# Optimization experiments

Hardware: AMD Instinct MI355X
Metric: run time of the kernel (lower is better)

## Reference

```python
import jax, jax.numpy as jnp
import numpy as np

HIDDEN = 384
HEADS = 8
DIM_HEAD = HIDDEN // HEADS  # 48
INNER = DIM_HEAD * HEADS
SCALE = DIM_HEAD ** -0.5


def setup_inputs() -> dict:
    key = jax.random.key(0)
    k1, k2, k3, k4 = jax.random.split(key, 4)
    B, C, D, H, W = 2, HIDDEN, 16, 16, 8
    x = jax.random.normal(k1, (B, C, D, H, W), dtype=jnp.float32)
    # nn.Linear weights (stored as [out, in] in torch; use [in, out] here)
    w_qkv = jax.random.normal(k2, (C, 3 * INNER), dtype=jnp.float32) * (C ** -0.5)
    w_out = jax.random.normal(k3, (INNER, C), dtype=jnp.float32) * (INNER ** -0.5)
    b_out = jax.random.normal(k4, (C,), dtype=jnp.float32) * 0.02
    return {"x": x, "w_qkv": w_qkv, "w_out": w_out, "b_out": b_out}


def reference(x, w_qkv, w_out, b_out):
    B, C, D, H, W = x.shape
    N = D * H * W
    tokens = x.reshape(B, C, N).transpose(0, 2, 1)          # [B, N, C]
    qkv = tokens @ w_qkv                                     # [B, N, 3*inner]
    qkv = qkv.reshape(B, N, 3, HEADS, DIM_HEAD).transpose(2, 0, 3, 1, 4)
    q, k, v = qkv[0], qkv[1], qkv[2]                         # [B, h, N, dh]
    q = jnp.clip(q, -5.0, 5.0)
    k = jnp.clip(k, -5.0, 5.0)
    logits = jnp.einsum('bhnd,bhmd->bhnm', q, k) * SCALE     # [B, h, N, N]
    logits = logits - jnp.max(logits, axis=-1, keepdims=True)
    attn = jax.nn.softmax(logits, axis=-1)
    out = jnp.einsum('bhnm,bhmd->bhnd', attn, v)             # [B, h, N, dh]
    out = out.transpose(0, 2, 1, 3).reshape(B, N, INNER)     # [B, N, inner]
    out = out @ w_out + b_out                                # [B, N, C]
    out = out.transpose(0, 2, 1).reshape(B, C, D, H, W)
    return x + out
```

## Files before the change

kernel.cpp:

```cpp
#include <hip/hip_runtime.h>

#define B_SZ 2
#define C_IN 384
#define N_TOK 2048
#define HEADS 8
#define DH 48
#define J3 1152
#define ATTN_SCALE 0.14433756729740643f

typedef __attribute__((ext_vector_type(8))) _Float16 f16x8;
typedef __attribute__((ext_vector_type(4))) _Float16 f16x4;
typedef __attribute__((ext_vector_type(4))) float f32x4;

__device__ __forceinline__ unsigned short f2h(float f) {
  _Float16 h = (_Float16)f;
  return __builtin_bit_cast(unsigned short, h);
}
__device__ __forceinline__ uint pk2(float a, float b) {
  return __builtin_bit_cast(uint, __builtin_amdgcn_cvt_pkrtz(a, b));
}

__global__ __launch_bounds__(256) void tr_kernel(
    const float* __restrict__ x, const float* __restrict__ wq,
    const float* __restrict__ wo, unsigned short* __restrict__ xh,
    unsigned short* __restrict__ wqh, unsigned short* __restrict__ woh) {
  const int z = blockIdx.z;
  const float* src;
  unsigned short* dst;
  int C;
  if (z < 2) {
    src = x + (size_t)z * C_IN * N_TOK;
    dst = xh + (size_t)z * N_TOK * C_IN;
    C = N_TOK;
  } else if (z == 2) {
    src = wq; dst = wqh; C = J3;
  } else {
    src = wo; dst = woh; C = C_IN;
  }
  const int c0 = blockIdx.x * 64;
  const int r0 = blockIdx.y * 64;
  if (c0 >= C) return;
  __shared__ unsigned short T[64][74];
  const int tid = threadIdx.x;
  const int cc = tid & 63;
#pragma unroll
  for (int i = 0; i < 16; ++i) {
    const int rr = 4 * i + (tid >> 6);
    T[cc][rr] = f2h(src[(size_t)(r0 + rr) * C + c0 + cc]);
  }
  __syncthreads();
  const int cc2 = tid >> 2;
  const int seg = (tid & 3) * 16;
  uint v[8];
#pragma unroll
  for (int k = 0; k < 8; ++k)
    v[k] = (uint)T[cc2][seg + 2 * k] | ((uint)T[cc2][seg + 2 * k + 1] << 16);
  unsigned short* dp = dst + (size_t)(c0 + cc2) * C_IN + r0 + seg;
  *(uint4*)dp = make_uint4(v[0], v[1], v[2], v[3]);
  *(uint4*)(dp + 8) = make_uint4(v[4], v[5], v[6], v[7]);
}

__global__ __launch_bounds__(256) void qkv_mfma(
    const unsigned short* __restrict__ xh, const unsigned short* __restrict__ wqh,
    unsigned short* __restrict__ Qo, unsigned short* __restrict__ Ko,
    unsigned short* __restrict__ Vo) {
  __shared__ __align__(16) unsigned short Ts[128][72];
  __shared__ __align__(16) unsigned short Ws[64][72];
  const int tid = threadIdx.x;
  const int w = tid >> 6, lane = tid & 63;
  const int lc = lane & 15, lg = lane >> 4;
  const int m0 = blockIdx.x * 128;
  const int j0 = blockIdx.y * 64;
  const int b = m0 >> 11;

  f32x4 acc[2][4];
#pragma unroll
  for (int i = 0; i < 2; ++i)
#pragma unroll
    for (int j = 0; j < 4; ++j) acc[i][j] = (f32x4){0.f, 0.f, 0.f, 0.f};

  const int trow = tid & 127, tseg = tid >> 7;
  const int wrow = tid & 63,  wseg = tid >> 6;

  for (int kk = 0; kk < C_IN; kk += 64) {
    {
      const uint4* s = (const uint4*)(xh + (size_t)(m0 + trow) * C_IN + kk + tseg * 32);
      uint4* d = (uint4*)&Ts[trow][tseg * 32];
      d[0] = s[0]; d[1] = s[1]; d[2] = s[2]; d[3] = s[3];
      const uint4* s2 = (const uint4*)(wqh + (size_t)(j0 + wrow) * C_IN + kk + wseg * 16);
      uint4* d2 = (uint4*)&Ws[wrow][wseg * 16];
      d2[0] = s2[0]; d2[1] = s2[1];
    }
    __syncthreads();
    f16x8 a[2][2], bf[4][2];
#pragma unroll
    for (int mt = 0; mt < 2; ++mt)
#pragma unroll
      for (int kh = 0; kh < 2; ++kh)
        a[mt][kh] = *(const f16x8*)&Ts[32 * w + 16 * mt + lc][32 * kh + 8 * lg];
#pragma unroll
    for (int jt = 0; jt < 4; ++jt)
#pragma unroll
      for (int kh = 0; kh < 2; ++kh)
        bf[jt][kh] = *(const f16x8*)&Ws[16 * jt + lc][32 * kh + 8 * lg];
#pragma unroll
    for (int mt = 0; mt < 2; ++mt)
#pragma unroll
      for (int jt = 0; jt < 4; ++jt)
#pragma unroll
        for (int kh = 0; kh < 2; ++kh)
          acc[mt][jt] = __builtin_amdgcn_mfma_f32_16x16x32_f16(a[mt][kh], bf[jt][kh], acc[mt][jt], 0, 0, 0);
    __syncthreads();
  }

#pragma unroll
  for (int jt = 0; jt < 4; ++jt) {
    const int jlo = j0 + 16 * jt;
    const int which = jlo / 384;
    const int rr = jlo - which * 384;
    const int head = rr / DH;
    const int dbase = rr - head * DH;
    const int d = dbase + lc;
    const int bh = b * HEADS + head;
#pragma unroll
    for (int mt = 0; mt < 2; ++mt)
#pragma unroll
      for (int r = 0; r < 4; ++r) {
        const int n = (m0 + 32 * w + 16 * mt + 4 * lg + r) & 2047;
        float val = acc[mt][jt][r];
        if (which == 0) {
          val = fminf(fmaxf(val, -5.f), 5.f) * ATTN_SCALE;
          Qo[((size_t)bh * N_TOK + n) * DH + d] = f2h(val);
        } else if (which == 1) {
          val = fminf(fmaxf(val, -5.f), 5.f);
          Ko[((size_t)bh * N_TOK + n) * DH + d] = f2h(val);
        } else {
          Vo[((size_t)bh * DH + d) * N_TOK + n] = f2h(val);
        }
      }
  }
}

__global__ __launch_bounds__(512) void attn_kernel(
    const unsigned short* __restrict__ Q, const unsigned short* __restrict__ K,
    const unsigned short* __restrict__ Vt, unsigned short* __restrict__ Opart,
    float2* __restrict__ ml) {
  const int qt = blockIdx.x, bh = blockIdx.y, ks = blockIdx.z;
  const int b = bh >> 3, h = bh & 7;
  const int n0 = qt * 128;
  const int tid = threadIdx.x;
  const int w = tid >> 6, lane = tid & 63;
  const int lc = lane & 15, lg = lane >> 4;

  __shared__ __align__(16) unsigned short Ks[64][56];
  __shared__ __align__(16) unsigned short Vs[48][68];

  const unsigned short* Qrow = Q + ((size_t)bh * N_TOK + n0 + 16 * w + lc) * DH;
  const f16x8 qf0 = *(const f16x8*)(Qrow + 8 * lg);
  f16x8 qf1 = {0, 0, 0, 0, 0, 0, 0, 0};
  {
    const f16x4 t = *(const f16x4*)(Qrow + 32 + 4 * lg);
    qf1[0] = t[0]; qf1[1] = t[1]; qf1[2] = t[2]; qf1[3] = t[3];
  }

  const unsigned short* Kg = K + (size_t)bh * N_TOK * DH + (size_t)ks * 1024 * DH;
  const uint* Vg32 = (const uint*)(Vt + (size_t)bh * DH * N_TOK) + ks * 512;

  float m_run = -1e30f, l_run = 0.f;
  f32x4 oacc[3] = {{0,0,0,0},{0,0,0,0},{0,0,0,0}};

  for (int t0 = 0; t0 < 1024; t0 += 64) {
    const uint* Ksrc = (const uint*)(Kg + (size_t)t0 * DH);
#pragma unroll
    for (int i = 0; i < 3; ++i) {
      const int dw = tid + i * 512;
      const int key = dw / 24, c = dw - key * 24;
      *(uint*)&Ks[key][2 * c] = Ksrc[dw];
      const int d = dw >> 5, c2 = dw & 31;
      *(uint*)&Vs[d][2 * c2] = Vg32[(size_t)d * 1024 + (t0 >> 1) + c2];
    }
    __syncthreads();

    f32x4 sac[4];
#pragma unroll
    for (int it = 0; it < 4; ++it) {
      const int krow = 16 * it + lc;
      const f16x8 kf0 = *(const f16x8*)&Ks[krow][8 * lg];
      f16x8 kf1 = {0, 0, 0, 0, 0, 0, 0, 0};
      const f16x4 t = *(const f16x4*)&Ks[krow][32 + 4 * lg];
      kf1[0] = t[0]; kf1[1] = t[1]; kf1[2] = t[2]; kf1[3] = t[3];
      const f32x4 z = {0.f, 0.f, 0.f, 0.f};
      f32x4 s = __builtin_amdgcn_mfma_f32_16x16x32_f16(kf0, qf0, z, 0, 0, 0);
      sac[it]  = __builtin_amdgcn_mfma_f32_16x16x32_f16(kf1, qf1, s, 0, 0, 0);
    }

    float mt = -1e30f;
#pragma unroll
    for (int it = 0; it < 4; ++it)
#pragma unroll
      for (int r = 0; r < 4; ++r) mt = fmaxf(mt, sac[it][r]);
    mt = fmaxf(mt, __shfl_xor(mt, 16, 64));
    mt = fmaxf(mt, __shfl_xor(mt, 32, 64));
    const float mn = fmaxf(m_run, mt);
    const float rs = __expf(m_run - mn);
    m_run = mn;
    float p[4][4];
    float ps = 0.f;
#pragma unroll
    for (int it = 0; it < 4; ++it)
#pragma unroll
      for (int r = 0; r < 4; ++r) {
        p[it][r] = __expf(sac[it][r] - mn);
        ps += p[it][r];
      }
    ps += __shfl_xor(ps, 16, 64);
    ps += __shfl_xor(ps, 32, 64);
    l_run = l_run * rs + ps;
#pragma unroll
    for (int itd = 0; itd < 3; ++itd)
#pragma unroll
      for (int r = 0; r < 4; ++r) oacc[itd][r] *= rs;

    f16x8 pt[2];
#pragma unroll
    for (int ks2 = 0; ks2 < 2; ++ks2) {
      union { f16x8 v; uint u[4]; } pu;
      pu.u[0] = pk2(p[2 * ks2][0], p[2 * ks2][1]);
      pu.u[1] = pk2(p[2 * ks2][2], p[2 * ks2][3]);
      pu.u[2] = pk2(p[2 * ks2 + 1][0], p[2 * ks2 + 1][1]);
      pu.u[3] = pk2(p[2 * ks2 + 1][2], p[2 * ks2 + 1][3]);
      pt[ks2] = pu.v;
    }

#pragma unroll
    for (int itd = 0; itd < 3; ++itd) {
      const int drow = 16 * itd + lc;
#pragma unroll
      for (int ks2 = 0; ks2 < 2; ++ks2) {
        const f16x4 v0 = *(const f16x4*)&Vs[drow][4 * lg + 32 * ks2];
        const f16x4 v1 = *(const f16x4*)&Vs[drow][4 * lg + 32 * ks2 + 16];
        f16x8 vf;
        vf[0] = v0[0]; vf[1] = v0[1]; vf[2] = v0[2]; vf[3] = v0[3];
        vf[4] = v1[0]; vf[5] = v1[1]; vf[6] = v1[2]; vf[7] = v1[3];
        oacc[itd] = __builtin_amdgcn_mfma_f32_16x16x32_f16(vf, pt[ks2], oacc[itd], 0, 0, 0);
      }
    }
    __syncthreads();
  }

  if (lg == 0)
    ml[(size_t)(ks * 16 + bh) * N_TOK + n0 + 16 * w + lc] = make_float2(m_run, l_run);
  unsigned short* Ap = Opart +
      ((size_t)(ks * B_SZ + b) * N_TOK + n0 + 16 * w + lc) * 384 + h * DH;
#pragma unroll
  for (int itd = 0; itd < 3; ++itd) {
    uint2 pkv;
    pkv.x = pk2(oacc[itd][0], oacc[itd][1]);
    pkv.y = pk2(oacc[itd][2], oacc[itd][3]);
    *(uint2*)(Ap + 16 * itd + 4 * lg) = pkv;
  }
}

__global__ __launch_bounds__(256) void combine_kernel(
    const unsigned short* __restrict__ Opart, const float2* __restrict__ ml,
    unsigned short* __restrict__ AOh) {
  const int vid = blockIdx.x * 256 + threadIdx.x;
  const int c8 = vid % 48;
  const int n  = (vid / 48) & 2047;
  const int b  = vid / (48 * 2048);
  const int c0 = c8 * 8;
  const int h  = c0 / 48;
  const int bh = b * 8 + h;
  const float2 ml1 = ml[(size_t)bh * N_TOK + n];
  const float2 ml2 = ml[(size_t)(16 + bh) * N_TOK + n];
  const float m = fmaxf(ml1.x, ml2.x);
  const float w1 = __expf(ml1.x - m), w2 = __expf(ml2.x - m);
  const float inv = 1.f / (ml1.y * w1 + ml2.y * w2);
  const float s1 = w1 * inv, s2 = w2 * inv;
  const size_t o1 = ((size_t)b * N_TOK + n) * 384 + c0;
  const size_t o2 = o1 + (size_t)B_SZ * N_TOK * 384;
  union { uint4 q; _Float16 e[8]; } u1, u2, r;
  u1.q = *(const uint4*)(Opart + o1);
  u2.q = *(const uint4*)(Opart + o2);
#pragma unroll
  for (int k = 0; k < 8; k += 2) {
    const float a = (float)u1.e[k] * s1 + (float)u2.e[k] * s2;
    const float bb = (float)u1.e[k + 1] * s1 + (float)u2.e[k + 1] * s2;
    *(uint*)&r.e[k] = pk2(a, bb);
  }
  *(uint4*)(AOh + o1) = r.q;
}

__global__ __launch_bounds__(256) void proj_mfma(
    const unsigned short* __restrict__ AOh, const unsigned short* __restrict__ woh,
    const float* __restrict__ b_out, const float* __restrict__ x,
    float* __restrict__ out) {
  __shared__ __align__(16) unsigned short As[64][72];
  __shared__ __align__(16) unsigned short Bs[128][72];
  const int tid = threadIdx.x;
  const int w = tid >> 6, lane = tid & 63;
  const int lc = lane & 15, lg = lane >> 4;
  const int c0 = blockIdx.x * 64;
  const int m0 = blockIdx.y * 128;
  const int b = m0 >> 11;

  f32x4 acc[4][2];
#pragma unroll
  for (int i = 0; i < 4; ++i)
#pragma unroll
    for (int j = 0; j < 2; ++j) acc[i][j] = (f32x4){0.f, 0.f, 0.f, 0.f};

  const int arow = tid & 63,  aseg = tid >> 6;
  const int brow = tid & 127, bseg = tid >> 7;

  for (int kk = 0; kk < C_IN; kk += 64) {
    {
      const uint4* s = (const uint4*)(woh + (size_t)(c0 + arow) * C_IN + kk + aseg * 16);
      uint4* d = (uint4*)&As[arow][aseg * 16];
      d[0] = s[0]; d[1] = s[1];
      const uint4* s2 = (const uint4*)(AOh + (size_t)(m0 + brow) * C_IN + kk + bseg * 32);
      uint4* d2 = (uint4*)&Bs[brow][bseg * 32];
      d2[0] = s2[0]; d2[1] = s2[1]; d2[2] = s2[2]; d2[3] = s2[3];
    }
    __syncthreads();
    f16x8 a[4][2], bf[2][2];
#pragma unroll
    for (int ct = 0; ct < 4; ++ct)
#pragma unroll
      for (int kh = 0; kh < 2; ++kh)
        a[ct][kh] = *(const f16x8*)&As[16 * ct + lc][32 * kh + 8 * lg];
#pragma unroll
    for (int mt = 0; mt < 2; ++mt)
#pragma unroll
      for (int kh = 0; kh < 2; ++kh)
        bf[mt][kh] = *(const f16x8*)&Bs[32 * w + 16 * mt + lc][32 * kh + 8 * lg];
#pragma unroll
    for (int ct = 0; ct < 4; ++ct)
#pragma unroll
      for (int mt = 0; mt < 2; ++mt)
#pragma unroll
        for (int kh = 0; kh < 2; ++kh)
          acc[ct][mt] = __builtin_amdgcn_mfma_f32_16x16x32_f16(a[ct][kh], bf[mt][kh], acc[ct][mt], 0, 0, 0);
    __syncthreads();
  }

#pragma unroll
  for (int ct = 0; ct < 4; ++ct)
#pragma unroll
    for (int r = 0; r < 4; ++r) {
      const int c = c0 + 16 * ct + 4 * lg + r;
      const float bias = b_out[c];
#pragma unroll
      for (int mt = 0; mt < 2; ++mt) {
        const int n = (m0 + 32 * w + 16 * mt + lc) & 2047;
        const size_t off = ((size_t)b * C_IN + c) * N_TOK + n;
        out[off] = x[off] + bias + acc[ct][mt][r];
      }
    }
}

extern "C" void kernel_launch(void* const* d_in, const int* in_sizes, int n_in,
                              void* d_out, int out_size, void* d_ws, size_t ws_size,
                              hipStream_t stream) {
  const float* x     = (const float*)d_in[0];
  const float* w_qkv = (const float*)d_in[1];
  const float* w_out = (const float*)d_in[2];
  const float* b_out = (const float*)d_in[3];
  float* out = (float*)d_out;

  char* ws = (char*)d_ws;
  unsigned short* xh    = (unsigned short*)(ws);
  unsigned short* wqh   = (unsigned short*)(ws + 3145728);
  unsigned short* woh   = (unsigned short*)(ws + 4030464);
  unsigned short* Qb    = (unsigned short*)(ws + 4325376);
  unsigned short* Kb    = (unsigned short*)(ws + 7471104);
  unsigned short* Vb    = (unsigned short*)(ws + 10616832);
  unsigned short* AOh   = (unsigned short*)(ws + 13762560);
  unsigned short* Opart = (unsigned short*)(ws + 16908288);
  float2*         mlb   = (float2*)(ws + 23199744);

  tr_kernel<<<dim3(32, 6, 4), 256, 0, stream>>>(x, w_qkv, w_out, xh, wqh, woh);
  qkv_mfma<<<dim3(32, 18), 256, 0, stream>>>(xh, wqh, Qb, Kb, Vb);
  attn_kernel<<<dim3(16, 16, 2), 512, 0, stream>>>(Qb, Kb, Vb, Opart, mlb);
  combine_kernel<<<dim3(768), 256, 0, stream>>>(Opart, mlb, AOh);
  proj_mfma<<<dim3(6, 32), 256, 0, stream>>>(AOh, woh, b_out, x, out);
}
```

Before: 81.61 us.

## Split attention keys four ways, double-buffer K/V, fuse combine into projection

Raises the key split of the attention kernel from 2 to 4 so more blocks run at once. K/V tiles are now prefetched into registers and written to a second shared-memory buffer, so global loads overlap compute and one barrier per tile is dropped. The separate combine kernel is removed: the projection GEMM merges the four partial outputs using per-row softmax weights while it loads its B tile. This saves a launch and the AOh round trip, but each projection block now rereads four partial buffers, repeating that work for every output-column block, and the attention partial writes double.

```diff
diff --git a/kernel.cpp b/kernel.cpp
--- a/kernel.cpp
+++ b/kernel.cpp
@@ -7,6 +7,8 @@
 #define DH 48
 #define J3 1152
 #define ATTN_SCALE 0.14433756729740643f
+#define KSPLIT 4
+#define KEYS_PER_SPLIT 512
 
 typedef __attribute__((ext_vector_type(8))) _Float16 f16x8;
 typedef __attribute__((ext_vector_type(4))) _Float16 f16x4;
@@ -152,8 +154,8 @@
   const int w = tid >> 6, lane = tid & 63;
   const int lc = lane & 15, lg = lane >> 4;
 
-  __shared__ __align__(16) unsigned short Ks[64][56];
-  __shared__ __align__(16) unsigned short Vs[48][68];
+  __shared__ __align__(16) unsigned short Ks[2][64][56];
+  __shared__ __align__(16) unsigned short Vs[2][48][68];
 
   const unsigned short* Qrow = Q + ((size_t)bh * N_TOK + n0 + 16 * w + lc) * DH;
   const f16x8 qf0 = *(const f16x8*)(Qrow + 8 * lg);
@@ -163,32 +165,48 @@
     qf1[0] = t[0]; qf1[1] = t[1]; qf1[2] = t[2]; qf1[3] = t[3];
   }
 
-  const unsigned short* Kg = K + (size_t)bh * N_TOK * DH + (size_t)ks * 1024 * DH;
-  const uint* Vg32 = (const uint*)(Vt + (size_t)bh * DH * N_TOK) + ks * 512;
-
-  float m_run = -1e30f, l_run = 0.f;
-  f32x4 oacc[3] = {{0,0,0,0},{0,0,0,0},{0,0,0,0}};
-
-  for (int t0 = 0; t0 < 1024; t0 += 64) {
+  const unsigned short* Kg = K + (size_t)bh * N_TOK * DH + (size_t)ks * KEYS_PER_SPLIT * DH;
+  const uint* Vg32 = (const uint*)(Vt + (size_t)bh * DH * N_TOK) + ks * (KEYS_PER_SPLIT / 2);
+
+  uint kr[3], vr[3];
+  auto issue = [&](int t0) {
     const uint* Ksrc = (const uint*)(Kg + (size_t)t0 * DH);
+#pragma unroll
+    for (int i = 0; i < 3; ++i) {
+      const int dw = tid + i * 512;
+      kr[i] = Ksrc[dw];
+      vr[i] = Vg32[(size_t)(dw >> 5) * 1024 + (t0 >> 1) + (dw & 31)];
+    }
+  };
+  auto commit = [&](int buf) {
 #pragma unroll
     for (int i = 0; i < 3; ++i) {
       const int dw = tid + i * 512;
       const int key = dw / 24, c = dw - key * 24;
-      *(uint*)&Ks[key][2 * c] = Ksrc[dw];
-      const int d = dw >> 5, c2 = dw & 31;
-      *(uint*)&Vs[d][2 * c2] = Vg32[(size_t)d * 1024 + (t0 >> 1) + c2];
-    }
+      *(uint*)&Ks[buf][key][2 * c] = kr[i];
+      *(uint*)&Vs[buf][dw >> 5][2 * (dw & 31)] = vr[i];
+    }
+  };
+
+  float m_run = -1e30f, l_run = 0.f;
+  f32x4 oacc[3] = {{0,0,0,0},{0,0,0,0},{0,0,0,0}};
+
+  issue(0);
+  commit(0);
+
+  for (int t = 0; t < KEYS_PER_SPLIT / 64; ++t) {
+    const int cur = t & 1;
+    if (t < KEYS_PER_SPLIT / 64 - 1) issue((t + 1) * 64);
     __syncthreads();
 
     f32x4 sac[4];
 #pragma unroll
     for (int it = 0; it < 4; ++it) {
       const int krow = 16 * it + lc;
-      const f16x8 kf0 = *(const f16x8*)&Ks[krow][8 * lg];
+      const f16x8 kf0 = *(const f16x8*)&Ks[cur][krow][8 * lg];
       f16x8 kf1 = {0, 0, 0, 0, 0, 0, 0, 0};
-      const f16x4 t = *(const f16x4*)&Ks[krow][32 + 4 * lg];
-      kf1[0] = t[0]; kf1[1] = t[1]; kf1[2] = t[2]; kf1[3] = t[3];
+      const f16x4 tt = *(const f16x4*)&Ks[cur][krow][32 + 4 * lg];
+      kf1[0] = tt[0]; kf1[1] = tt[1]; kf1[2] = tt[2]; kf1[3] = tt[3];
       const f32x4 z = {0.f, 0.f, 0.f, 0.f};
       f32x4 s = __builtin_amdgcn_mfma_f32_16x16x32_f16(kf0, qf0, z, 0, 0, 0);
       sac[it]  = __builtin_amdgcn_mfma_f32_16x16x32_f16(kf1, qf1, s, 0, 0, 0);
@@ -237,15 +255,16 @@
       const int drow = 16 * itd + lc;
 #pragma unroll
       for (int ks2 = 0; ks2 < 2; ++ks2) {
-        const f16x4 v0 = *(const f16x4*)&Vs[drow][4 * lg + 32 * ks2];
-        const f16x4 v1 = *(const f16x4*)&Vs[drow][4 * lg + 32 * ks2 + 16];
+        const f16x4 v0 = *(const f16x4*)&Vs[cur][drow][4 * lg + 32 * ks2];
+        const f16x4 v1 = *(const f16x4*)&Vs[cur][drow][4 * lg + 32 * ks2 + 16];
         f16x8 vf;
         vf[0] = v0[0]; vf[1] = v0[1]; vf[2] = v0[2]; vf[3] = v0[3];
         vf[4] = v1[0]; vf[5] = v1[1]; vf[6] = v1[2]; vf[7] = v1[3];
         oacc[itd] = __builtin_amdgcn_mfma_f32_16x16x32_f16(vf, pt[ks2], oacc[itd], 0, 0, 0);
       }
     }
-    __syncthreads();
+
+    if (t < KEYS_PER_SPLIT / 64 - 1) commit(cur ^ 1);
   }
 
   if (lg == 0)
@@ -261,48 +280,38 @@
   }
 }
 
-__global__ __launch_bounds__(256) void combine_kernel(
+__global__ __launch_bounds__(256) void proj_mfma(
     const unsigned short* __restrict__ Opart, const float2* __restrict__ ml,
-    unsigned short* __restrict__ AOh) {
-  const int vid = blockIdx.x * 256 + threadIdx.x;
-  const int c8 = vid % 48;
-  const int n  = (vid / 48) & 2047;
-  const int b  = vid / (48 * 2048);
-  const int c0 = c8 * 8;
-  const int h  = c0 / 48;
-  const int bh = b * 8 + h;
-  const float2 ml1 = ml[(size_t)bh * N_TOK + n];
-  const float2 ml2 = ml[(size_t)(16 + bh) * N_TOK + n];
-  const float m = fmaxf(ml1.x, ml2.x);
-  const float w1 = __expf(ml1.x - m), w2 = __expf(ml2.x - m);
-  const float inv = 1.f / (ml1.y * w1 + ml2.y * w2);
-  const float s1 = w1 * inv, s2 = w2 * inv;
-  const size_t o1 = ((size_t)b * N_TOK + n) * 384 + c0;
-  const size_t o2 = o1 + (size_t)B_SZ * N_TOK * 384;
-  union { uint4 q; _Float16 e[8]; } u1, u2, r;
-  u1.q = *(const uint4*)(Opart + o1);
-  u2.q = *(const uint4*)(Opart + o2);
-#pragma unroll
-  for (int k = 0; k < 8; k += 2) {
-    const float a = (float)u1.e[k] * s1 + (float)u2.e[k] * s2;
-    const float bb = (float)u1.e[k + 1] * s1 + (float)u2.e[k + 1] * s2;
-    *(uint*)&r.e[k] = pk2(a, bb);
-  }
-  *(uint4*)(AOh + o1) = r.q;
-}
-
-__global__ __launch_bounds__(256) void proj_mfma(
-    const unsigned short* __restrict__ AOh, const unsigned short* __restrict__ woh,
-    const float* __restrict__ b_out, const float* __restrict__ x,
-    float* __restrict__ out) {
+    const unsigned short* __restrict__ woh, const float* __restrict__ b_out,
+    const float* __restrict__ x, float* __restrict__ out) {
   __shared__ __align__(16) unsigned short As[64][72];
   __shared__ __align__(16) unsigned short Bs[128][72];
+  __shared__ float4 SW[128][8];
   const int tid = threadIdx.x;
   const int w = tid >> 6, lane = tid & 63;
   const int lc = lane & 15, lg = lane >> 4;
   const int c0 = blockIdx.x * 64;
   const int m0 = blockIdx.y * 128;
   const int b = m0 >> 11;
+  const size_t PS = (size_t)B_SZ * N_TOK * 384;
+
+#pragma unroll
+  for (int i = 0; i < 4; ++i) {
+    const int idx = tid + i * 256;
+    const int mm = idx >> 3, hh = idx & 7;
+    const int n = (m0 + mm) & 2047;
+    const int bh = b * 8 + hh;
+    const float2 e0 = ml[(size_t)(0 * 16 + bh) * N_TOK + n];
+    const float2 e1 = ml[(size_t)(1 * 16 + bh) * N_TOK + n];
+    const float2 e2 = ml[(size_t)(2 * 16 + bh) * N_TOK + n];
+    const float2 e3 = ml[(size_t)(3 * 16 + bh) * N_TOK + n];
+    const float M = fmaxf(fmaxf(e0.x, e1.x), fmaxf(e2.x, e3.x));
+    const float w0 = __expf(e0.x - M), w1 = __expf(e1.x - M);
+    const float w2 = __expf(e2.x - M), w3 = __expf(e3.x - M);
+    const float inv = 1.f / (w0 * e0.y + w1 * e1.y + w2 * e2.y + w3 * e3.y);
+    SW[mm][hh] = make_float4(w0 * inv, w1 * inv, w2 * inv, w3 * inv);
+  }
+  __syncthreads();
 
   f32x4 acc[4][2];
 #pragma unroll
@@ -312,15 +321,34 @@
 
   const int arow = tid & 63,  aseg = tid >> 6;
   const int brow = tid & 127, bseg = tid >> 7;
+  const int bn = (m0 + brow) & 2047;
 
   for (int kk = 0; kk < C_IN; kk += 64) {
     {
       const uint4* s = (const uint4*)(woh + (size_t)(c0 + arow) * C_IN + kk + aseg * 16);
       uint4* d = (uint4*)&As[arow][aseg * 16];
       d[0] = s[0]; d[1] = s[1];
-      const uint4* s2 = (const uint4*)(AOh + (size_t)(m0 + brow) * C_IN + kk + bseg * 32);
-      uint4* d2 = (uint4*)&Bs[brow][bseg * 32];
-      d2[0] = s2[0]; d2[1] = s2[1]; d2[2] = s2[2]; d2[3] = s2[3];
+      const size_t ro = ((size_t)b * N_TOK + bn) * 384 + kk + bseg * 32;
+      union U8 { uint4 q; _Float16 e[8]; };
+#pragma unroll
+      for (int sseg = 0; sseg < 4; ++sseg) {
+        const int ce = kk + bseg * 32 + sseg * 8;
+        const float4 s4 = SW[brow][ce / 48];
+        U8 u0, u1, u2, u3, r;
+        u0.q = *(const uint4*)(Opart + 0 * PS + ro + sseg * 8);
+        u1.q = *(const uint4*)(Opart + 1 * PS + ro + sseg * 8);
+        u2.q = *(const uint4*)(Opart + 2 * PS + ro + sseg * 8);
+        u3.q = *(const uint4*)(Opart + 3 * PS + ro + sseg * 8);
+#pragma unroll
+        for (int e = 0; e < 8; e += 2) {
+          const float va = (float)u0.e[e] * s4.x + (float)u1.e[e] * s4.y +
+                           (float)u2.e[e] * s4.z + (float)u3.e[e] * s4.w;
+          const float vb = (float)u0.e[e + 1] * s4.x + (float)u1.e[e + 1] * s4.y +
+                           (float)u2.e[e + 1] * s4.z + (float)u3.e[e + 1] * s4.w;
+          *(uint*)&r.e[e] = pk2(va, vb);
+        }
+        *(uint4*)&Bs[brow][bseg * 32 + sseg * 8] = r.q;
+      }
     }
     __syncthreads();
     f16x8 a[4][2], bf[2][2];
@@ -375,13 +403,11 @@
   unsigned short* Qb    = (unsigned short*)(ws + 4325376);
   unsigned short* Kb    = (unsigned short*)(ws + 7471104);
   unsigned short* Vb    = (unsigned short*)(ws + 10616832);
-  unsigned short* AOh   = (unsigned short*)(ws + 13762560);
-  unsigned short* Opart = (unsigned short*)(ws + 16908288);
-  float2*         mlb   = (float2*)(ws + 23199744);
+  unsigned short* Opart = (unsigned short*)(ws + 13762560);
+  float2*         mlb   = (float2*)(ws + 26345472);
 
   tr_kernel<<<dim3(32, 6, 4), 256, 0, stream>>>(x, w_qkv, w_out, xh, wqh, woh);
   qkv_mfma<<<dim3(32, 18), 256, 0, stream>>>(xh, wqh, Qb, Kb, Vb);
-  attn_kernel<<<dim3(16, 16, 2), 512, 0, stream>>>(Qb, Kb, Vb, Opart, mlb);
-  combine_kernel<<<dim3(768), 256, 0, stream>>>(Opart, mlb, AOh);
-  proj_mfma<<<dim3(6, 32), 256, 0, stream>>>(AOh, woh, b_out, x, out);
-}
+  attn_kernel<<<dim3(16, 16, KSPLIT), 512, 0, stream>>>(Qb, Kb, Vb, Opart, mlb);
+  proj_mfma<<<dim3(6, 32), 256, 0, stream>>>(Opart, mlb, woh, b_out, x, out);
+}
```

Result: slower. 89.79 us (+10.0%).
